# Performance work log

Measured on AMD Instinct MI355X. Metric: run time of the kernel, lower is better.

Reference implementation:

```python
import jax, jax.numpy as jnp
import numpy as np

H = 128
NH = 8  # num attention heads


def _ln(x, g, b, eps=1e-5):
    m = x.mean(-1, keepdims=True)
    v = ((x - m) ** 2).mean(-1, keepdims=True)
    return (x - m) / jnp.sqrt(v + eps) * g + b


def _mha(q_in, kv_in, Wqkv, bqkv, Wo, bo):
    # torch nn.MultiheadAttention with packed in_proj, batch=1, eval (no dropout)
    h = q_in.shape[-1]
    hd = h // NH
    Wq, Wk, Wv = Wqkv[:h], Wqkv[h:2 * h], Wqkv[2 * h:]
    bq, bk, bv = bqkv[:h], bqkv[h:2 * h], bqkv[2 * h:]
    q = (q_in @ Wq.T + bq).reshape(-1, NH, hd).transpose(1, 0, 2)   # [nh, Nq, hd]
    k = (kv_in @ Wk.T + bk).reshape(-1, NH, hd).transpose(1, 0, 2)  # [nh, Nk, hd]
    v = (kv_in @ Wv.T + bv).reshape(-1, NH, hd).transpose(1, 0, 2)
    scores = jnp.einsum('hqd,hkd->hqk', q, k) / jnp.sqrt(jnp.asarray(hd, q.dtype))
    attn = jax.nn.softmax(scores, axis=-1)
    out = jnp.einsum('hqk,hkd->hqd', attn, v)                       # [nh, Nq, hd]
    out = out.transpose(1, 0, 2).reshape(-1, h)
    return out @ Wo.T + bo


def setup_inputs() -> dict:
    key = jax.random.key(0)
    ks = jax.random.split(key, 32)
    s = 0.05
    d = {
        'ligand_features': jax.random.normal(ks[0], (512, 128), jnp.float32),
        'pocket_features': jax.random.normal(ks[1], (1024, 128), jnp.float32),
        'ligand_coords': jax.random.uniform(ks[2], (512, 3), jnp.float32) * 20.0,
        'pocket_coords': jax.random.uniform(ks[3], (1024, 3), jnp.float32) * 20.0,
        # projections
        'Wl': jax.random.normal(ks[4], (H, 128), jnp.float32) * s,
        'bl': jnp.zeros((H,), jnp.float32),
        'Wp': jax.random.normal(ks[5], (H, 128), jnp.float32) * s,
        'bp': jnp.zeros((H,), jnp.float32),
        # distance encoder: 1 -> h/4 -> h/2 -> h
        'Wd1': jax.random.normal(ks[6], (H // 4, 1), jnp.float32) * s,
        'bd1': jnp.zeros((H // 4,), jnp.float32),
        'Wd2': jax.random.normal(ks[7], (H // 2, H // 4), jnp.float32) * s,
        'bd2': jnp.zeros((H // 2,), jnp.float32),
        'Wd3': jax.random.normal(ks[8], (H, H // 2), jnp.float32) * s,
        'bd3': jnp.zeros((H,), jnp.float32),
        # gates
        'Wgl': jax.random.normal(ks[9], (H, 2 * H), jnp.float32) * s,
        'bgl': jnp.zeros((H,), jnp.float32),
        'Wgp': jax.random.normal(ks[10], (H, 2 * H), jnp.float32) * s,
        'bgp': jnp.zeros((H,), jnp.float32),
        # shared cross-attention (packed qkv like torch)
        'Wqkv': jax.random.normal(ks[11], (3 * H, H), jnp.float32) * s,
        'bqkv': jnp.zeros((3 * H,), jnp.float32),
        'Wo': jax.random.normal(ks[12], (H, H), jnp.float32) * s,
        'bo': jnp.zeros((H,), jnp.float32),
        # layer norms
        'g_l': jnp.ones((H,), jnp.float32),
        'be_l': jnp.zeros((H,), jnp.float32),
        'g_p': jnp.ones((H,), jnp.float32),
        'be_p': jnp.zeros((H,), jnp.float32),
    }
    return d


def reference(ligand_features, pocket_features, ligand_coords, pocket_coords,
              Wl, bl, Wp, bp, Wd1, bd1, Wd2, bd2, Wd3, bd3,
              Wgl, bgl, Wgp, bgp, Wqkv, bqkv, Wo, bo,
              g_l, be_l, g_p, be_p):
    lig = ligand_features @ Wl.T + bl   # [Nl, H]
    poc = pocket_features @ Wp.T + bp   # [Np, H]

    # pairwise distances [Nl, Np]
    diff = ligand_coords[:, None, :] - pocket_coords[None, :, :]
    dist = jnp.sqrt(jnp.sum(diff * diff, axis=-1))

    # distance encoder MLP applied elementwise -> [Nl, Np, H]
    e = jax.nn.relu(dist[..., None] @ Wd1.T + bd1)
    e = jax.nn.relu(e @ Wd2.T + bd2)
    enc = e @ Wd3.T + bd3
    m = enc.mean(axis=-1)               # [Nl, Np]

    # ligand enhancement: softmax over pocket axis
    sw_l = jax.nn.softmax(-m, axis=-1)          # [Nl, Np]
    agg_l = sw_l @ poc                          # [Nl, H]
    gate_l = jax.nn.sigmoid(jnp.concatenate([lig, agg_l], axis=-1) @ Wgl.T + bgl)
    lig_enh = gate_l * lig + (1.0 - gate_l) * agg_l

    # pocket enhancement: transposed encoding, softmax over ligand axis
    sw_p = jax.nn.softmax(-m.T, axis=-1)        # [Np, Nl]
    agg_p = sw_p @ lig                          # [Np, H]
    gate_p = jax.nn.sigmoid(jnp.concatenate([poc, agg_p], axis=-1) @ Wgp.T + bgp)
    poc_enh = gate_p * poc + (1.0 - gate_p) * agg_p

    lig_att = _mha(lig_enh, poc_enh, Wqkv, bqkv, Wo, bo)
    poc_att = _mha(poc_enh, lig_enh, Wqkv, bqkv, Wo, bo)

    lig_fused = _ln(lig_enh + lig_att, g_l, be_l)
    poc_fused = _ln(poc_enh + poc_att, g_p, be_p)
    return (lig_fused, poc_fused)
```

## Files before the change

### kernel.cpp

```cpp
#include <hip/hip_runtime.h>
#include <math.h>

#define NL 512
#define NP 1024
#define HDIM 128

#define TAB_N 8192
#define DMAX 34.65f

#define M_OFF    128
#define WLT_OFF  (M_OFF)
#define WPT_OFF  (M_OFF + 16384)
#define WQT_OFF  (M_OFF + 32768)
#define WOT_OFF  (M_OFF + 81920)
#define WGLT_OFF (M_OFF + 98304)
#define WGPT_OFF (M_OFF + 131072)
#define TAB_OFF  (M_OFF + 163840)
#define LIG_OFF  (M_OFF + NL*NP)
#define POC_OFF  (LIG_OFF + NL*HDIM)
#define LENH_OFF (POC_OFF + NP*HDIM)
#define PENH_OFF (LENH_OFF + NL*HDIM)
#define QKVL_OFF (PENH_OFF + NP*HDIM)
#define QKVP_OFF (QKVL_OFF + NL*384)
#define PARTL_OFF (QKVP_OFF + NP*384)
#define PARTP_OFF (PARTL_OFF + 512*8*8*18)

__device__ __forceinline__ float dot4f(float4 a, float4 b){
  return fmaf(a.x,b.x, fmaf(a.y,b.y, fmaf(a.z,b.z, a.w*b.w)));
}

__device__ __forceinline__ void tpose(const float* __restrict__ src, float* __restrict__ dst,
                                      int O, int K, int blk0, int t){
  int e0 = blk0*1024 + t*4;
  #pragma unroll
  for (int i = 0; i < 4; i++){
    int e = e0 + i;
    int o = e / K, k = e - o*K;
    dst[(size_t)k*O + o] = src[(size_t)o*K + k];
  }
}
__global__ __launch_bounds__(256) void prep_all(const float* __restrict__ Wl, const float* __restrict__ Wp,
                                                const float* __restrict__ Wqkv, const float* __restrict__ Wo,
                                                const float* __restrict__ Wgl, const float* __restrict__ Wgp,
                                                const float* __restrict__ Wd1, const float* __restrict__ bd1,
                                                const float* __restrict__ Wd2, const float* __restrict__ bd2,
                                                const float* __restrict__ Wd3, const float* __restrict__ bd3,
                                                float* __restrict__ ws){
  int b = blockIdx.x, t = threadIdx.x;
  if (b < 160){
    if      (b < 16)  tpose(Wl,   ws + WLT_OFF,  128, 128, b,       t);
    else if (b < 32)  tpose(Wp,   ws + WPT_OFF,  128, 128, b - 16,  t);
    else if (b < 80)  tpose(Wqkv, ws + WQT_OFF,  384, 128, b - 32,  t);
    else if (b < 96)  tpose(Wo,   ws + WOT_OFF,  128, 128, b - 80,  t);
    else if (b < 128) tpose(Wgl,  ws + WGLT_OFF, 128, 256, b - 96,  t);
    else              tpose(Wgp,  ws + WGPT_OFF, 128, 256, b - 128, t);
    return;
  }
  float* tab = ws + TAB_OFF;
  __shared__ float sWd1[32], sbd1[32], sWd2[2048], sbd2[64], swd3m[64];
  __shared__ float sbd3m;
  int idx = (b - 160) * 256 + t;
  if (t < 64){
    float s = 0.f;
    #pragma unroll 8
    for (int i = 0; i < 128; i++) s += Wd3[i*64 + t];
    swd3m[t] = s * (1.f/128.f);
  } else if (t == 64){
    float s = 0.f;
    for (int i = 0; i < 128; i++) s += bd3[i];
    sbd3m = s * (1.f/128.f);
  } else if (t >= 128 && t < 160){ sWd1[t-128] = Wd1[t-128]; sbd1[t-128] = bd1[t-128]; }
  else if (t >= 160 && t < 224){ sbd2[t-160] = bd2[t-160]; }
  for (int k = t; k < 2048; k += 256) sWd2[k] = Wd2[k];
  __syncthreads();

  float d = (float)idx * (DMAX / (float)(TAB_N - 1));
  float4 e1q[8];
  const float4* w1q = (const float4*)sWd1;
  const float4* b1q = (const float4*)sbd1;
  #pragma unroll
  for (int k4 = 0; k4 < 8; k4++){
    float4 w = w1q[k4], bb = b1q[k4];
    float4 e;
    e.x = fmaxf(fmaf(d, w.x, bb.x), 0.f);
    e.y = fmaxf(fmaf(d, w.y, bb.y), 0.f);
    e.z = fmaxf(fmaf(d, w.z, bb.z), 0.f);
    e.w = fmaxf(fmaf(d, w.w, bb.w), 0.f);
    e1q[k4] = e;
  }
  float mv = sbd3m;
  #pragma unroll 4
  for (int j2 = 0; j2 < 64; j2++){
    const float4* wrow = (const float4*)(sWd2 + j2*32);
    float a0 = 0.f, a1 = 0.f, a2 = 0.f, a3 = 0.f;
    #pragma unroll
    for (int k4 = 0; k4 < 8; k4++){
      float4 w = wrow[k4], e = e1q[k4];
      a0 = fmaf(w.x, e.x, a0);
      a1 = fmaf(w.y, e.y, a1);
      a2 = fmaf(w.z, e.z, a2);
      a3 = fmaf(w.w, e.w, a3);
    }
    float e2v = fmaxf(sbd2[j2] + ((a0+a1)+(a2+a3)), 0.f);
    mv = fmaf(swd3m[j2], e2v, mv);
  }
  tab[idx] = mv;
}

__global__ __launch_bounds__(256) void proj_kernel(const float* __restrict__ lf, const float* __restrict__ pf,
                                                   const float* __restrict__ WlT, const float* __restrict__ bl,
                                                   const float* __restrict__ WpT, const float* __restrict__ bp,
                                                   float* __restrict__ lig, float* __restrict__ poc){
  int b = blockIdx.x, t = threadIdx.x;
  bool isLig = (b < NL/2);
  int r0 = isLig ? b*2 : (b - NL/2)*2;
  const float* in = (isLig ? lf : pf) + (size_t)r0*HDIM;
  const float* WT = isLig ? WlT : WpT;
  const float* bias = isLig ? bl : bp;
  float* out = (isLig ? lig : poc) + (size_t)r0*HDIM;
  __shared__ float sx[2*HDIM];
  sx[t] = in[t];
  __syncthreads();
  int r = t >> 7, col = t & 127;
  const float* xr = sx + r*HDIM;
  float acc = bias[col];
  #pragma unroll 8
  for (int k = 0; k < 128; k++) acc = fmaf(WT[k*128 + col], xr[k], acc);
  out[r*HDIM + col] = acc;
}

__global__ __launch_bounds__(512) void agg_gate_fused(const float* __restrict__ lc, const float* __restrict__ pc,
                                                      const float* __restrict__ tab,
                                                      const float* __restrict__ lig, const float* __restrict__ poc,
                                                      const float* __restrict__ WglT, const float* __restrict__ bgl,
                                                      const float* __restrict__ WgpT, const float* __restrict__ bgp,
                                                      const float* __restrict__ WqkvT, const float* __restrict__ bqkv,
                                                      float* __restrict__ lenh, float* __restrict__ penh,
                                                      float* __restrict__ qkvl, float* __restrict__ qkvp){
  int b = blockIdx.x, t = threadIdx.x;
  bool isLig = (b < NL/2);
  int r0 = isLig ? b*2 : (b - NL/2)*2;
  int n = isLig ? NP : NL;
  const float* myFeat = isLig ? lig : poc;
  const float* otherFeat = isLig ? poc : lig;
  const float* myC = isLig ? lc : pc;
  const float* otC = isLig ? pc : lc;

  __shared__ float w[2*NP];
  __shared__ float sx[2*HDIM];
  __shared__ float sa[2*HDIM];
  __shared__ float4 part4[8*64];
  __shared__ float gpart[512];
  __shared__ float redm[8];
  __shared__ float sgm[2], sinv[2];

  int rr = t >> 8, u = t & 255;
  int lane = t & 63, wv = t >> 6;
  int row = r0 + rr;

  if (t < 256) sx[t] = myFeat[(size_t)r0*HDIM + t];

  float cx = myC[row*3+0], cy = myC[row*3+1], cz = myC[row*3+2];
  const float inv_h = (float)(TAB_N - 1) / DMAX;
  int per = n >> 8;

  float xs[4];
  float lmax = -1e30f;
  for (int k = 0; k < per; k++){
    int j = u + (k << 8);
    float ox = otC[j*3+0], oy = otC[j*3+1], oz = otC[j*3+2];
    float dx = cx-ox, dy = cy-oy, dz = cz-oz;
    float d = sqrtf(fmaf(dx,dx, fmaf(dy,dy, dz*dz)));
    float xf = d * inv_h;
    int i0 = (int)xf;
    i0 = (i0 > TAB_N-2) ? (TAB_N-2) : i0;
    float f = xf - (float)i0;
    float v0 = tab[i0], v1 = tab[i0+1];
    xs[k] = -fmaf(f, v1 - v0, v0);
    lmax = fmaxf(lmax, xs[k]);
  }
  float v = lmax;
  #pragma unroll
  for (int off = 32; off; off >>= 1) v = fmaxf(v, __shfl_down(v, off));
  if (lane == 0) redm[wv] = v;
  __syncthreads();
  if (t < 2) sgm[t] = fmaxf(fmaxf(redm[t*4+0], redm[t*4+1]), fmaxf(redm[t*4+2], redm[t*4+3]));
  __syncthreads();
  float gm = sgm[rr];
  float lsum = 0.f;
  for (int k = 0; k < per; k++){
    float e = __expf(xs[k] - gm);
    w[rr*NP + u + (k << 8)] = e;
    lsum += e;
  }
  v = lsum;
  #pragma unroll
  for (int off = 32; off; off >>= 1) v += __shfl_down(v, off);
  if (lane == 0) redm[wv] = v;
  __syncthreads();
  if (t < 2) sinv[t] = 1.0f / ((redm[t*4+0] + redm[t*4+1]) + (redm[t*4+2] + redm[t*4+3]));
  __syncthreads();

  {
    int jg = t >> 6;
    int r  = (t >> 5) & 1;
    int c4 = t & 31;
    int per2 = n >> 3;
    int jb0 = jg * per2;
    const float4* of4 = (const float4*)otherFeat;
    const float* wR = w + r*NP;
    float4 acc = {0,0,0,0};
    #pragma unroll 4
    for (int jj = 0; jj < per2; jj++){
      int j = jb0 + jj;
      float4 f = of4[(size_t)j*32 + c4];
      float ww = wR[j];
      acc.x = fmaf(ww, f.x, acc.x); acc.y = fmaf(ww, f.y, acc.y);
      acc.z = fmaf(ww, f.z, acc.z); acc.w = fmaf(ww, f.w, acc.w);
    }
    part4[(jg*2 + r)*32 + c4] = acc;
  }
  __syncthreads();
  #pragma unroll
  for (int s = 4; s >= 1; s >>= 1){
    if (t < s*64){
      int g2 = t >> 6, rem = t & 63;
      float4 a = part4[g2*64 + rem], bb = part4[(g2+s)*64 + rem];
      a.x += bb.x; a.y += bb.y; a.z += bb.z; a.w += bb.w;
      part4[g2*64 + rem] = a;
    }
    __syncthreads();
  }
  if (t < 256) sa[t] = ((const float*)part4)[t] * sinv[t >> 7];
  __syncthreads();

  {
    int r  = t >> 8;
    int kg = (t >> 7) & 1;
    int col = t & 127;
    const float* WT = isLig ? WglT : WgpT;
    const float* inq = (kg == 0) ? (sx + r*HDIM) : (sa + r*HDIM);
    const float* wbase = WT + (size_t)kg*128*128;
    float g = 0.f;
    #pragma unroll 8
    for (int k = 0; k < 128; k++) g = fmaf(wbase[k*128 + col], inq[k], g);
    gpart[kg*256 + r*128 + col] = g;
  }
  __syncthreads();
  float enh_val = 0.f;
  if (t < 256){
    int r = t >> 7, col = t & 127;
    const float* bg = isLig ? bgl : bgp;
    float g = bg[col] + gpart[t] + gpart[256 + t];
    g = 1.0f / (1.0f + __expf(-g));
    float xv = sx[t], av = sa[t];
    enh_val = fmaf(g, xv - av, av);
    float* dst = isLig ? (lenh + (size_t)(r0+r)*HDIM) : (penh + (size_t)(r0+r)*HDIM);
    dst[col] = enh_val;
  }
  __syncthreads();
  if (t < 256) sa[t] = enh_val;
  __syncthreads();

  {
    int r = t >> 8, ln = t & 255;
    const float* er = sa + r*HDIM;
    float* qout = (isLig ? qkvl : qkvp) + (size_t)(r0+r)*384;
    if (ln < 128){
      float a0 = bqkv[ln], a2 = bqkv[ln+256];
      #pragma unroll 4
      for (int k = 0; k < 128; k++){
        float xv = er[k];
        const float* wk = WqkvT + k*384;
        a0 = fmaf(wk[ln],     xv, a0);
        a2 = fmaf(wk[ln+256], xv, a2);
      }
      qout[ln] = a0; qout[ln+256] = a2;
    } else {
      float a1 = bqkv[ln];
      #pragma unroll 4
      for (int k = 0; k < 128; k++) a1 = fmaf(WqkvT[k*384 + ln], er[k], a1);
      qout[ln] = a1;
    }
  }
}

__global__ __launch_bounds__(256) void attn_part(const float* __restrict__ qkvl, const float* __restrict__ qkvp,
                                                 float* __restrict__ partL, float* __restrict__ partP){
  int bx = blockIdx.x;
  int t = threadIdx.x;
  const float* qsrc; const float* kvsrc; int qt, slice; bool isLig;
  if (bx < 256){ isLig = true;  qt = bx >> 3; slice = bx & 7; qsrc = qkvl; kvsrc = qkvp; }
  else { int b2 = bx - 256; isLig = false; qt = b2 >> 2; slice = b2 & 3; qsrc = qkvp; kvsrc = qkvl; }
  int g = t >> 6, tt = t & 63;
  int h = tt >> 3, qp = tt & 7;
  int j0 = slice*128 + g*32;

  const float4* qA = (const float4*)(qsrc + (size_t)(qt*16+qp)*384 + h*16);
  const float4* qB = (const float4*)(qsrc + (size_t)(qt*16+qp+8)*384 + h*16);
  float4 a0 = qA[0], a1 = qA[1], a2 = qA[2], a3 = qA[3];
  float4 b0 = qB[0], b1 = qB[1], b2 = qB[2], b3 = qB[3];
  float mA = -1e30f, lA = 0.f, mB = -1e30f, lB = 0.f;
  float4 OA0={0,0,0,0}, OA1={0,0,0,0}, OA2={0,0,0,0}, OA3={0,0,0,0};
  float4 OB0={0,0,0,0}, OB1={0,0,0,0}, OB2={0,0,0,0}, OB3={0,0,0,0};

  __shared__ float sKV[8192];
  float* myKV = sKV + g*2048;

  for (int tile = 0; tile < 4; tile++){
    int jbase = j0 + tile*8;
    __syncthreads();
    #pragma unroll
    for (int nn = 0; nn < 8; nn++){
      int v4 = tt + nn*64;
      int jj = v4 >> 6, c4 = v4 & 63;
      ((float4*)myKV)[jj*64 + c4] = *(const float4*)(kvsrc + (size_t)(jbase+jj)*384 + 128 + c4*4);
    }
    __syncthreads();
    float sA[8], sB[8];
    #pragma unroll
    for (int jj = 0; jj < 8; jj++){
      const float4* kk = (const float4*)(myKV + jj*256 + h*16);
      float4 k0 = kk[0], k1 = kk[1], k2 = kk[2], k3 = kk[3];
      sA[jj] = (dot4f(a0,k0) + dot4f(a1,k1) + dot4f(a2,k2) + dot4f(a3,k3)) * 0.25f;
      sB[jj] = (dot4f(b0,k0) + dot4f(b1,k1) + dot4f(b2,k2) + dot4f(b3,k3)) * 0.25f;
    }
    float mtA = sA[0], mtB = sB[0];
    #pragma unroll
    for (int jj = 1; jj < 8; jj++){ mtA = fmaxf(mtA, sA[jj]); mtB = fmaxf(mtB, sB[jj]); }
    float mnA = fmaxf(mA, mtA), mnB = fmaxf(mB, mtB);
    float cA = __expf(mA - mnA), cB = __expf(mB - mnB);
    lA *= cA; lB *= cB;
    OA0.x*=cA; OA0.y*=cA; OA0.z*=cA; OA0.w*=cA;
    OA1.x*=cA; OA1.y*=cA; OA1.z*=cA; OA1.w*=cA;
    OA2.x*=cA; OA2.y*=cA; OA2.z*=cA; OA2.w*=cA;
    OA3.x*=cA; OA3.y*=cA; OA3.z*=cA; OA3.w*=cA;
    OB0.x*=cB; OB0.y*=cB; OB0.z*=cB; OB0.w*=cB;
    OB1.x*=cB; OB1.y*=cB; OB1.z*=cB; OB1.w*=cB;
    OB2.x*=cB; OB2.y*=cB; OB2.z*=cB; OB2.w*=cB;
    OB3.x*=cB; OB3.y*=cB; OB3.z*=cB; OB3.w*=cB;
    #pragma unroll
    for (int jj = 0; jj < 8; jj++){
      float pA = __expf(sA[jj] - mnA);
      float pB = __expf(sB[jj] - mnB);
      lA += pA; lB += pB;
      const float4* vv = (const float4*)(myKV + jj*256 + 128 + h*16);
      float4 v0 = vv[0], v1 = vv[1], v2 = vv[2], v3 = vv[3];
      OA0.x = fmaf(pA, v0.x, OA0.x); OA0.y = fmaf(pA, v0.y, OA0.y);
      OA0.z = fmaf(pA, v0.z, OA0.z); OA0.w = fmaf(pA, v0.w, OA0.w);
      OA1.x = fmaf(pA, v1.x, OA1.x); OA1.y = fmaf(pA, v1.y, OA1.y);
      OA1.z = fmaf(pA, v1.z, OA1.z); OA1.w = fmaf(pA, v1.w, OA1.w);
      OA2.x = fmaf(pA, v2.x, OA2.x); OA2.y = fmaf(pA, v2.y, OA2.y);
      OA2.z = fmaf(pA, v2.z, OA2.z); OA2.w = fmaf(pA, v2.w, OA2.w);
      OA3.x = fmaf(pA, v3.x, OA3.x); OA3.y = fmaf(pA, v3.y, OA3.y);
      OA3.z = fmaf(pA, v3.z, OA3.z); OA3.w = fmaf(pA, v3.w, OA3.w);
      OB0.x = fmaf(pB, v0.x, OB0.x); OB0.y = fmaf(pB, v0.y, OB0.y);
      OB0.z = fmaf(pB, v0.z, OB0.z); OB0.w = fmaf(pB, v0.w, OB0.w);
      OB1.x = fmaf(pB, v1.x, OB1.x); OB1.y = fmaf(pB, v1.y, OB1.y);
      OB1.z = fmaf(pB, v1.z, OB1.z); OB1.w = fmaf(pB, v1.w, OB1.w);
      OB2.x = fmaf(pB, v2.x, OB2.x); OB2.y = fmaf(pB, v2.y, OB2.y);
      OB2.z = fmaf(pB, v2.z, OB2.z); OB2.w = fmaf(pB, v2.w, OB2.w);
      OB3.x = fmaf(pB, v3.x, OB3.x); OB3.y = fmaf(pB, v3.y, OB3.y);
      OB3.z = fmaf(pB, v3.z, OB3.z); OB3.w = fmaf(pB, v3.w, OB3.w);
    }
    mA = mnA; mB = mnB;
  }

  __syncthreads();
  if (g > 0){
    float* bA = sKV + (size_t)((g-1)*128 + tt*2)*19;
    bA[0]=mA; bA[1]=lA;
    bA[2]=OA0.x; bA[3]=OA0.y; bA[4]=OA0.z; bA[5]=OA0.w;
    bA[6]=OA1.x; bA[7]=OA1.y; bA[8]=OA1.z; bA[9]=OA1.w;
    bA[10]=OA2.x; bA[11]=OA2.y; bA[12]=OA2.z; bA[13]=OA2.w;
    bA[14]=OA3.x; bA[15]=OA3.y; bA[16]=OA3.z; bA[17]=OA3.w;
    float* bB = bA + 19;
    bB[0]=mB; bB[1]=lB;
    bB[2]=OB0.x; bB[3]=OB0.y; bB[4]=OB0.z; bB[5]=OB0.w;
    bB[6]=OB1.x; bB[7]=OB1.y; bB[8]=OB1.z; bB[9]=OB1.w;
    bB[10]=OB2.x; bB[11]=OB2.y; bB[12]=OB2.z; bB[13]=OB2.w;
    bB[14]=OB3.x; bB[15]=OB3.y; bB[16]=OB3.z; bB[17]=OB3.w;
  }
  __syncthreads();
  if (g == 0){
    float M = mA, L = lA;
    float O[16] = {OA0.x,OA0.y,OA0.z,OA0.w, OA1.x,OA1.y,OA1.z,OA1.w,
                   OA2.x,OA2.y,OA2.z,OA2.w, OA3.x,OA3.y,OA3.z,OA3.w};
    #pragma unroll
    for (int gg = 1; gg < 4; gg++){
      const float* br = sKV + (size_t)((gg-1)*128 + tt*2)*19;
      float m1 = br[0], l1 = br[1];
      float Mn = fmaxf(M, m1);
      float e0 = __expf(M - Mn), e1 = __expf(m1 - Mn);
      L = L*e0 + l1*e1;
      #pragma unroll
      for (int k = 0; k < 16; k++) O[k] = O[k]*e0 + br[2+k]*e1;
      M = Mn;
    }
    int rowA = qt*16 + qp;
    float* dst = isLig ? (partL + ((size_t)(rowA*8 + h)*8 + slice)*18)
                       : (partP + ((size_t)(rowA*8 + h)*4 + slice)*18);
    dst[0] = M; dst[1] = L;
    #pragma unroll
    for (int k = 0; k < 16; k++) dst[2+k] = O[k];
    M = mB; L = lB;
    float Ob[16] = {OB0.x,OB0.y,OB0.z,OB0.w, OB1.x,OB1.y,OB1.z,OB1.w,
                    OB2.x,OB2.y,OB2.z,OB2.w, OB3.x,OB3.y,OB3.z,OB3.w};
    #pragma unroll
    for (int gg = 1; gg < 4; gg++){
      const float* br = sKV + (size_t)((gg-1)*128 + tt*2 + 1)*19;
      float m1 = br[0], l1 = br[1];
      float Mn = fmaxf(M, m1);
      float e0 = __expf(M - Mn), e1 = __expf(m1 - Mn);
      L = L*e0 + l1*e1;
      #pragma unroll
      for (int k = 0; k < 16; k++) Ob[k] = Ob[k]*e0 + br[2+k]*e1;
      M = Mn;
    }
    int rowB = qt*16 + qp + 8;
    float* dstB = isLig ? (partL + ((size_t)(rowB*8 + h)*8 + slice)*18)
                        : (partP + ((size_t)(rowB*8 + h)*4 + slice)*18);
    dstB[0] = M; dstB[1] = L;
    #pragma unroll
    for (int k = 0; k < 16; k++) dstB[2+k] = Ob[k];
  }
}

__global__ __launch_bounds__(256) void merge_ln(const float* __restrict__ partL, const float* __restrict__ partP,
                                                const float* __restrict__ lenh, const float* __restrict__ penh,
                                                const float* __restrict__ WoT, const float* __restrict__ bo,
                                                const float* __restrict__ g_l, const float* __restrict__ be_l,
                                                const float* __restrict__ g_p, const float* __restrict__ be_p,
                                                float* __restrict__ out){
  int b = blockIdx.x, t = threadIdx.x;
  int r0 = b*2;
  int r = t >> 7, c = t & 127;
  int gr = r0 + r;
  int h = c >> 4, cc = c & 15;
  int ns; const float* base;
  if (gr < NL){ ns = 8; base = partL + ((size_t)(gr*8 + h))*8*18; }
  else        { ns = 4; base = partP + ((size_t)((gr-NL)*8 + h))*4*18; }
  float M = -1e30f;
  for (int s = 0; s < ns; s++) M = fmaxf(M, base[s*18]);
  float Lsum = 0.f, Osum = 0.f;
  for (int s = 0; s < ns; s++){
    float e = __expf(base[s*18] - M);
    Lsum = fmaf(e, base[s*18+1], Lsum);
    Osum = fmaf(e, base[s*18+2+cc], Osum);
  }
  __shared__ float sAtt[2*HDIM];
  sAtt[t] = Osum / Lsum;
  __syncthreads();
  float o = bo[c];
  const float* sA = sAtt + r*HDIM;
  #pragma unroll 8
  for (int k = 0; k < 128; k++) o = fmaf(WoT[k*128 + c], sA[k], o);
  const float* enh = (gr < NL) ? (lenh + (size_t)gr*HDIM) : (penh + (size_t)(gr-NL)*HDIM);
  float x = enh[c] + o;
  __shared__ float sred[8];
  int wid = t >> 6;
  float v = x;
  #pragma unroll
  for (int off = 32; off; off >>= 1) v += __shfl_down(v, off);
  if ((t & 63) == 0) sred[wid] = v;
  __syncthreads();
  float mu = (sred[2*r] + sred[2*r+1]) * (1.f/128.f);
  float dx = x - mu;
  v = dx*dx;
  #pragma unroll
  for (int off = 32; off; off >>= 1) v += __shfl_down(v, off);
  if ((t & 63) == 0) sred[4 + wid] = v;
  __syncthreads();
  float var = (sred[4 + 2*r] + sred[4 + 2*r+1]) * (1.f/128.f);
  float y = dx * rsqrtf(var + 1e-5f);
  if (gr < NL) y = fmaf(y, g_l[c], be_l[c]);
  else         y = fmaf(y, g_p[c], be_p[c]);
  out[(size_t)gr*HDIM + c] = y;
}

extern "C" void kernel_launch(void* const* d_in, const int* in_sizes, int n_in,
                              void* d_out, int out_size, void* d_ws, size_t ws_size,
                              hipStream_t stream){
  const float* lf   = (const float*)d_in[0];
  const float* pf   = (const float*)d_in[1];
  const float* lc   = (const float*)d_in[2];
  const float* pc   = (const float*)d_in[3];
  const float* Wl   = (const float*)d_in[4];
  const float* bl   = (const float*)d_in[5];
  const float* Wp   = (const float*)d_in[6];
  const float* bp   = (const float*)d_in[7];
  const float* Wd1  = (const float*)d_in[8];
  const float* bd1  = (const float*)d_in[9];
  const float* Wd2  = (const float*)d_in[10];
  const float* bd2  = (const float*)d_in[11];
  const float* Wd3  = (const float*)d_in[12];
  const float* bd3  = (const float*)d_in[13];
  const float* Wgl  = (const float*)d_in[14];
  const float* bgl  = (const float*)d_in[15];
  const float* Wgp  = (const float*)d_in[16];
  const float* bgp  = (const float*)d_in[17];
  const float* Wqkv = (const float*)d_in[18];
  const float* bqkv = (const float*)d_in[19];
  const float* Wo   = (const float*)d_in[20];
  const float* bo   = (const float*)d_in[21];
  const float* g_l  = (const float*)d_in[22];
  const float* be_l = (const float*)d_in[23];
  const float* g_p  = (const float*)d_in[24];
  const float* be_p = (const float*)d_in[25];

  float* ws  = (float*)d_ws;
  float* out = (float*)d_out;
  float* lig   = ws + LIG_OFF;
  float* poc   = ws + POC_OFF;
  float* lenh  = ws + LENH_OFF;
  float* penh  = ws + PENH_OFF;
  float* qkvl  = ws + QKVL_OFF;
  float* qkvp  = ws + QKVP_OFF;
  float* partL = ws + PARTL_OFF;
  float* partP = ws + PARTP_OFF;
  float* tab   = ws + TAB_OFF;

  prep_all<<<192, 256, 0, stream>>>(Wl, Wp, Wqkv, Wo, Wgl, Wgp, Wd1, bd1, Wd2, bd2, Wd3, bd3, ws);
  proj_kernel<<<NL/2 + NP/2, 256, 0, stream>>>(lf, pf, ws + WLT_OFF, bl, ws + WPT_OFF, bp, lig, poc);
  agg_gate_fused<<<NL/2 + NP/2, 512, 0, stream>>>(lc, pc, tab, lig, poc,
                                                  ws + WGLT_OFF, bgl, ws + WGPT_OFF, bgp,
                                                  ws + WQT_OFF, bqkv,
                                                  lenh, penh, qkvl, qkvp);
  attn_part<<<512, 256, 0, stream>>>(qkvl, qkvp, partL, partP);
  merge_ln<<<NL/2 + NP/2, 256, 0, stream>>>(partL, partP, lenh, penh, ws + WOT_OFF, bo,
                                            g_l, be_l, g_p, be_p, out);
}
```

Baseline: 194.1 us.

## Process four query rows per thread in attention with 512-thread blocks

```diff
diff --git a/kernel.cpp b/kernel.cpp
--- a/kernel.cpp
+++ b/kernel.cpp
@@ -285,29 +285,37 @@
   }
 }
 
-__global__ __launch_bounds__(256) void attn_part(const float* __restrict__ qkvl, const float* __restrict__ qkvp,
+__global__ __launch_bounds__(512) void attn_part(const float* __restrict__ qkvl, const float* __restrict__ qkvp,
                                                  float* __restrict__ partL, float* __restrict__ partP){
   int bx = blockIdx.x;
   int t = threadIdx.x;
   const float* qsrc; const float* kvsrc; int qt, slice; bool isLig;
-  if (bx < 256){ isLig = true;  qt = bx >> 3; slice = bx & 7; qsrc = qkvl; kvsrc = qkvp; }
-  else { int b2 = bx - 256; isLig = false; qt = b2 >> 2; slice = b2 & 3; qsrc = qkvp; kvsrc = qkvl; }
+  if (bx < 128){ isLig = true;  qt = bx >> 3; slice = bx & 7; qsrc = qkvl; kvsrc = qkvp; }
+  else { int b2 = bx - 128; isLig = false; qt = b2 >> 2; slice = b2 & 3; qsrc = qkvp; kvsrc = qkvl; }
   int g = t >> 6, tt = t & 63;
   int h = tt >> 3, qp = tt & 7;
-  int j0 = slice*128 + g*32;
-
-  const float4* qA = (const float4*)(qsrc + (size_t)(qt*16+qp)*384 + h*16);
-  const float4* qB = (const float4*)(qsrc + (size_t)(qt*16+qp+8)*384 + h*16);
-  float4 a0 = qA[0], a1 = qA[1], a2 = qA[2], a3 = qA[3];
-  float4 b0 = qB[0], b1 = qB[1], b2 = qB[2], b3 = qB[3];
-  float mA = -1e30f, lA = 0.f, mB = -1e30f, lB = 0.f;
-  float4 OA0={0,0,0,0}, OA1={0,0,0,0}, OA2={0,0,0,0}, OA3={0,0,0,0};
-  float4 OB0={0,0,0,0}, OB1={0,0,0,0}, OB2={0,0,0,0}, OB3={0,0,0,0};
-
-  __shared__ float sKV[8192];
+  int j0 = slice*128 + g*16;
+  int rowbase = qt*32 + qp;
+
+  float4 qf[4][4];
+  #pragma unroll
+  for (int qi = 0; qi < 4; qi++){
+    const float4* qq = (const float4*)(qsrc + (size_t)(rowbase + qi*8)*384 + h*16);
+    qf[qi][0] = qq[0]; qf[qi][1] = qq[1]; qf[qi][2] = qq[2]; qf[qi][3] = qq[3];
+  }
+  float m[4], l[4];
+  float4 O[4][4];
+  #pragma unroll
+  for (int qi = 0; qi < 4; qi++){
+    m[qi] = -1e30f; l[qi] = 0.f;
+    #pragma unroll
+    for (int rr = 0; rr < 4; rr++) O[qi][rr] = make_float4(0.f,0.f,0.f,0.f);
+  }
+
+  __shared__ float sKV[16384];
   float* myKV = sKV + g*2048;
 
-  for (int tile = 0; tile < 4; tile++){
+  for (int tile = 0; tile < 2; tile++){
     int jbase = j0 + tile*8;
     __syncthreads();
     #pragma unroll
@@ -317,112 +325,90 @@
       ((float4*)myKV)[jj*64 + c4] = *(const float4*)(kvsrc + (size_t)(jbase+jj)*384 + 128 + c4*4);
     }
     __syncthreads();
-    float sA[8], sB[8];
+    float s[4][8];
     #pragma unroll
     for (int jj = 0; jj < 8; jj++){
       const float4* kk = (const float4*)(myKV + jj*256 + h*16);
       float4 k0 = kk[0], k1 = kk[1], k2 = kk[2], k3 = kk[3];
-      sA[jj] = (dot4f(a0,k0) + dot4f(a1,k1) + dot4f(a2,k2) + dot4f(a3,k3)) * 0.25f;
-      sB[jj] = (dot4f(b0,k0) + dot4f(b1,k1) + dot4f(b2,k2) + dot4f(b3,k3)) * 0.25f;
-    }
-    float mtA = sA[0], mtB = sB[0];
+      #pragma unroll
+      for (int qi = 0; qi < 4; qi++)
+        s[qi][jj] = (dot4f(qf[qi][0],k0) + dot4f(qf[qi][1],k1) +
+                     dot4f(qf[qi][2],k2) + dot4f(qf[qi][3],k3)) * 0.25f;
+    }
     #pragma unroll
-    for (int jj = 1; jj < 8; jj++){ mtA = fmaxf(mtA, sA[jj]); mtB = fmaxf(mtB, sB[jj]); }
-    float mnA = fmaxf(mA, mtA), mnB = fmaxf(mB, mtB);
-    float cA = __expf(mA - mnA), cB = __expf(mB - mnB);
-    lA *= cA; lB *= cB;
-    OA0.x*=cA; OA0.y*=cA; OA0.z*=cA; OA0.w*=cA;
-    OA1.x*=cA; OA1.y*=cA; OA1.z*=cA; OA1.w*=cA;
-    OA2.x*=cA; OA2.y*=cA; OA2.z*=cA; OA2.w*=cA;
-    OA3.x*=cA; OA3.y*=cA; OA3.z*=cA; OA3.w*=cA;
-    OB0.x*=cB; OB0.y*=cB; OB0.z*=cB; OB0.w*=cB;
-    OB1.x*=cB; OB1.y*=cB; OB1.z*=cB; OB1.w*=cB;
-    OB2.x*=cB; OB2.y*=cB; OB2.z*=cB; OB2.w*=cB;
-    OB3.x*=cB; OB3.y*=cB; OB3.z*=cB; OB3.w*=cB;
+    for (int qi = 0; qi < 4; qi++){
+      float mt = s[qi][0];
+      #pragma unroll
+      for (int jj = 1; jj < 8; jj++) mt = fmaxf(mt, s[qi][jj]);
+      float mn = fmaxf(m[qi], mt);
+      float c = __expf(m[qi] - mn);
+      l[qi] *= c;
+      #pragma unroll
+      for (int rr = 0; rr < 4; rr++){
+        O[qi][rr].x *= c; O[qi][rr].y *= c; O[qi][rr].z *= c; O[qi][rr].w *= c;
+      }
+      m[qi] = mn;
+      #pragma unroll
+      for (int jj = 0; jj < 8; jj++){
+        float p = __expf(s[qi][jj] - mn);
+        s[qi][jj] = p;
+        l[qi] += p;
+      }
+    }
     #pragma unroll
     for (int jj = 0; jj < 8; jj++){
-      float pA = __expf(sA[jj] - mnA);
-      float pB = __expf(sB[jj] - mnB);
-      lA += pA; lB += pB;
       const float4* vv = (const float4*)(myKV + jj*256 + 128 + h*16);
       float4 v0 = vv[0], v1 = vv[1], v2 = vv[2], v3 = vv[3];
-      OA0.x = fmaf(pA, v0.x, OA0.x); OA0.y = fmaf(pA, v0.y, OA0.y);
-      OA0.z = fmaf(pA, v0.z, OA0.z); OA0.w = fmaf(pA, v0.w, OA0.w);
-      OA1.x = fmaf(pA, v1.x, OA1.x); OA1.y = fmaf(pA, v1.y, OA1.y);
-      OA1.z = fmaf(pA, v1.z, OA1.z); OA1.w = fmaf(pA, v1.w, OA1.w);
-      OA2.x = fmaf(pA, v2.x, OA2.x); OA2.y = fmaf(pA, v2.y, OA2.y);
-      OA2.z = fmaf(pA, v2.z, OA2.z); OA2.w = fmaf(pA, v2.w, OA2.w);
-      OA3.x = fmaf(pA, v3.x, OA3.x); OA3.y = fmaf(pA, v3.y, OA3.y);
-      OA3.z = fmaf(pA, v3.z, OA3.z); OA3.w = fmaf(pA, v3.w, OA3.w);
-      OB0.x = fmaf(pB, v0.x, OB0.x); OB0.y = fmaf(pB, v0.y, OB0.y);
-      OB0.z = fmaf(pB, v0.z, OB0.z); OB0.w = fmaf(pB, v0.w, OB0.w);
-      OB1.x = fmaf(pB, v1.x, OB1.x); OB1.y = fmaf(pB, v1.y, OB1.y);
-      OB1.z = fmaf(pB, v1.z, OB1.z); OB1.w = fmaf(pB, v1.w, OB1.w);
-      OB2.x = fmaf(pB, v2.x, OB2.x); OB2.y = fmaf(pB, v2.y, OB2.y);
-      OB2.z = fmaf(pB, v2.z, OB2.z); OB2.w = fmaf(pB, v2.w, OB2.w);
-      OB3.x = fmaf(pB, v3.x, OB3.x); OB3.y = fmaf(pB, v3.y, OB3.y);
-      OB3.z = fmaf(pB, v3.z, OB3.z); OB3.w = fmaf(pB, v3.w, OB3.w);
-    }
-    mA = mnA; mB = mnB;
-  }
-
-  __syncthreads();
-  if (g > 0){
-    float* bA = sKV + (size_t)((g-1)*128 + tt*2)*19;
-    bA[0]=mA; bA[1]=lA;
-    bA[2]=OA0.x; bA[3]=OA0.y; bA[4]=OA0.z; bA[5]=OA0.w;
-    bA[6]=OA1.x; bA[7]=OA1.y; bA[8]=OA1.z; bA[9]=OA1.w;
-    bA[10]=OA2.x; bA[11]=OA2.y; bA[12]=OA2.z; bA[13]=OA2.w;
-    bA[14]=OA3.x; bA[15]=OA3.y; bA[16]=OA3.z; bA[17]=OA3.w;
-    float* bB = bA + 19;
-    bB[0]=mB; bB[1]=lB;
-    bB[2]=OB0.x; bB[3]=OB0.y; bB[4]=OB0.z; bB[5]=OB0.w;
-    bB[6]=OB1.x; bB[7]=OB1.y; bB[8]=OB1.z; bB[9]=OB1.w;
-    bB[10]=OB2.x; bB[11]=OB2.y; bB[12]=OB2.z; bB[13]=OB2.w;
-    bB[14]=OB3.x; bB[15]=OB3.y; bB[16]=OB3.z; bB[17]=OB3.w;
-  }
-  __syncthreads();
-  if (g == 0){
-    float M = mA, L = lA;
-    float O[16] = {OA0.x,OA0.y,OA0.z,OA0.w, OA1.x,OA1.y,OA1.z,OA1.w,
-                   OA2.x,OA2.y,OA2.z,OA2.w, OA3.x,OA3.y,OA3.z,OA3.w};
-    #pragma unroll
-    for (int gg = 1; gg < 4; gg++){
-      const float* br = sKV + (size_t)((gg-1)*128 + tt*2)*19;
-      float m1 = br[0], l1 = br[1];
-      float Mn = fmaxf(M, m1);
-      float e0 = __expf(M - Mn), e1 = __expf(m1 - Mn);
-      L = L*e0 + l1*e1;
-      #pragma unroll
-      for (int k = 0; k < 16; k++) O[k] = O[k]*e0 + br[2+k]*e1;
-      M = Mn;
-    }
-    int rowA = qt*16 + qp;
-    float* dst = isLig ? (partL + ((size_t)(rowA*8 + h)*8 + slice)*18)
-                       : (partP + ((size_t)(rowA*8 + h)*4 + slice)*18);
-    dst[0] = M; dst[1] = L;
-    #pragma unroll
-    for (int k = 0; k < 16; k++) dst[2+k] = O[k];
-    M = mB; L = lB;
-    float Ob[16] = {OB0.x,OB0.y,OB0.z,OB0.w, OB1.x,OB1.y,OB1.z,OB1.w,
-                    OB2.x,OB2.y,OB2.z,OB2.w, OB3.x,OB3.y,OB3.z,OB3.w};
-    #pragma unroll
-    for (int gg = 1; gg < 4; gg++){
-      const float* br = sKV + (size_t)((gg-1)*128 + tt*2 + 1)*19;
-      float m1 = br[0], l1 = br[1];
-      float Mn = fmaxf(M, m1);
-      float e0 = __expf(M - Mn), e1 = __expf(m1 - Mn);
-      L = L*e0 + l1*e1;
-      #pragma unroll
-      for (int k = 0; k < 16; k++) Ob[k] = Ob[k]*e0 + br[2+k]*e1;
-      M = Mn;
-    }
-    int rowB = qt*16 + qp + 8;
-    float* dstB = isLig ? (partL + ((size_t)(rowB*8 + h)*8 + slice)*18)
-                        : (partP + ((size_t)(rowB*8 + h)*4 + slice)*18);
-    dstB[0] = M; dstB[1] = L;
-    #pragma unroll
-    for (int k = 0; k < 16; k++) dstB[2+k] = Ob[k];
+      #pragma unroll
+      for (int qi = 0; qi < 4; qi++){
+        float p = s[qi][jj];
+        O[qi][0].x = fmaf(p, v0.x, O[qi][0].x); O[qi][0].y = fmaf(p, v0.y, O[qi][0].y);
+        O[qi][0].z = fmaf(p, v0.z, O[qi][0].z); O[qi][0].w = fmaf(p, v0.w, O[qi][0].w);
+        O[qi][1].x = fmaf(p, v1.x, O[qi][1].x); O[qi][1].y = fmaf(p, v1.y, O[qi][1].y);
+        O[qi][1].z = fmaf(p, v1.z, O[qi][1].z); O[qi][1].w = fmaf(p, v1.w, O[qi][1].w);
+        O[qi][2].x = fmaf(p, v2.x, O[qi][2].x); O[qi][2].y = fmaf(p, v2.y, O[qi][2].y);
+        O[qi][2].z = fmaf(p, v2.z, O[qi][2].z); O[qi][2].w = fmaf(p, v2.w, O[qi][2].w);
+        O[qi][3].x = fmaf(p, v3.x, O[qi][3].x); O[qi][3].y = fmaf(p, v3.y, O[qi][3].y);
+        O[qi][3].z = fmaf(p, v3.z, O[qi][3].z); O[qi][3].w = fmaf(p, v3.w, O[qi][3].w);
+      }
+    }
+  }
+
+  for (int qi = 0; qi < 4; qi++){
+    __syncthreads();
+    if (g > 0){
+      float* bb = sKV + (size_t)((g-1)*64 + tt)*19;
+      bb[0] = m[qi]; bb[1] = l[qi];
+      bb[2]  = O[qi][0].x; bb[3]  = O[qi][0].y; bb[4]  = O[qi][0].z; bb[5]  = O[qi][0].w;
+      bb[6]  = O[qi][1].x; bb[7]  = O[qi][1].y; bb[8]  = O[qi][1].z; bb[9]  = O[qi][1].w;
+      bb[10] = O[qi][2].x; bb[11] = O[qi][2].y; bb[12] = O[qi][2].z; bb[13] = O[qi][2].w;
+      bb[14] = O[qi][3].x; bb[15] = O[qi][3].y; bb[16] = O[qi][3].z; bb[17] = O[qi][3].w;
+    }
+    __syncthreads();
+    if (g == 0){
+      float M = m[qi], L = l[qi];
+      float Ov[16] = {O[qi][0].x,O[qi][0].y,O[qi][0].z,O[qi][0].w,
+                      O[qi][1].x,O[qi][1].y,O[qi][1].z,O[qi][1].w,
+                      O[qi][2].x,O[qi][2].y,O[qi][2].z,O[qi][2].w,
+                      O[qi][3].x,O[qi][3].y,O[qi][3].z,O[qi][3].w};
+      #pragma unroll
+      for (int gg = 1; gg < 8; gg++){
+        const float* br = sKV + (size_t)((gg-1)*64 + tt)*19;
+        float m1 = br[0], l1 = br[1];
+        float Mn = fmaxf(M, m1);
+        float e0 = __expf(M - Mn), e1 = __expf(m1 - Mn);
+        L = L*e0 + l1*e1;
+        #pragma unroll
+        for (int k = 0; k < 16; k++) Ov[k] = Ov[k]*e0 + br[2+k]*e1;
+        M = Mn;
+      }
+      int rowX = rowbase + qi*8;
+      float* dst = isLig ? (partL + ((size_t)(rowX*8 + h)*8 + slice)*18)
+                         : (partP + ((size_t)(rowX*8 + h)*4 + slice)*18);
+      dst[0] = M; dst[1] = L;
+      #pragma unroll
+      for (int k = 0; k < 16; k++) dst[2+k] = Ov[k];
+    }
   }
 }
 
@@ -526,7 +512,7 @@
                                                   ws + WGLT_OFF, bgl, ws + WGPT_OFF, bgp,
                                                   ws + WQT_OFF, bqkv,
                                                   lenh, penh, qkvl, qkvp);
-  attn_part<<<512, 256, 0, stream>>>(qkvl, qkvp, partL, partP);
+  attn_part<<<256, 512, 0, stream>>>(qkvl, qkvp, partL, partP);
   merge_ln<<<NL/2 + NP/2, 256, 0, stream>>>(partL, partP, lenh, penh, ws + WOT_OFF, bo,
                                             g_l, be_l, g_p, be_p, out);
 }
```

Measured after the change: 200.2 us. 1.03x slower.
